# Optimization experiments

Hardware: AMD Instinct MI355X
Metric: run time of the kernel (lower is better)

Reference implementation:

```python
import jax, jax.numpy as jnp
import numpy as np

# dims: B = clips*frames, L = x spatial tokens, C = input/output/linear_out dim,
# D = conv_dim_in, NV = conv_dim_out == linear_in (visual tokens), T = num_tk
B, L, C, D, NV, T, FR = 160, 196, 768, 512, 196, 87, 10
DM, DS = C // 2, C // 16          # affine bottleneck d_model, adapter down size
ALPHA, BETA, GAMMA = 0.3, 0.05, 0.05
EPS = 1e-5


def _ln(x, g, b):
    m = x.mean(-1, keepdims=True)
    v = jnp.mean((x - m) ** 2, axis=-1, keepdims=True)
    return (x - m) * jax.lax.rsqrt(v + EPS) * g + b


def _forward(x, vis_token, conv_w, conv_b, fc_w, fc_b, my_tokens, gate_av,
             a1_w, a1_b, v1_w, v1_b, bt_w, bt_b, vc_w, vc_b, v2_w, v2_b,
             a2_w, a2_b, vs_w, vs_b, tg_w, tg_b, lnb_g, lnb_b, down_w,
             bn1_g, bn1_b, bn1_m, bn1_v, up_w, bn2_g, bn2_b, bn2_m, bn2_v,
             lnp_g, lnp_b, gate):
    vt = vis_token[..., 0]                                   # (B,NV,D)
    # conv_adapter: 1x1 conv over channel axis D -> NV, then fc over token axis NV -> C
    h = jnp.einsum('od,bnd->bon', conv_w, vt) + conv_b[None, :, None]   # (B,NV,NV)
    V = jnp.einsum('bon,cn->boc', h, fc_w) + fc_b            # (B,NV,C)  == vis_token tokens

    # token <-> visual cross-attention
    rep = jnp.broadcast_to(my_tokens, (x.shape[0], T, C))    # (B,T,C)
    att_v2tk = jax.nn.softmax(jnp.einsum('btd,bnd->btn', rep, V), axis=-1)
    rep = rep + jnp.einsum('btn,bnd->btd', att_v2tk, V)

    xt = jnp.transpose(x[..., 0], (0, 2, 1))                 # (B,L,C)
    att_tk2x = jax.nn.softmax(jnp.einsum('bld,btd->blt', xt, rep), axis=-1)
    xt = xt + gate_av * jnp.einsum('blt,btd->bld', att_tk2x, rep)

    # channel attention
    audio = V.mean(axis=1)                                   # (B,C)
    aq1 = jax.nn.relu(audio @ a1_w.T + a1_b)[:, None, :]     # (B,1,C)
    vq1 = jax.nn.relu(xt @ v1_w.T + v1_b)                    # (B,L,C)
    avq = jax.nn.relu((aq1 * vq1).mean(axis=1) @ bt_w.T + bt_b)          # (B,DM)
    ch = jax.nn.sigmoid(avq @ vc_w.T + vc_b)[:, None, :]     # (B,1,C)
    cfeat = xt * (ch + 1.0)                                  # (B,L,C)

    # spatial attention
    cq = jax.nn.relu(cfeat @ v2_w.T + v2_b)                  # (B,L,DM)
    aq2 = jax.nn.relu(audio @ a2_w.T + a2_b)[:, None, :]     # (B,1,DM)
    s_tmp = (cq * aq2) @ vs_w.T + vs_b                       # (B,L,1)
    s_sig = jax.nn.sigmoid(s_tmp)                            # (B,L,1)
    spatial = jax.nn.softmax(jnp.tanh(s_tmp).transpose(0, 2, 1), axis=-1)  # (B,1,L)

    # temporal gate over frames
    audio_r = audio.reshape(B // FR, FR, C)
    temporal = jax.nn.sigmoid(audio_r @ tg_w.T + tg_b)[..., None]          # (bs,FR,1,1)

    x5 = xt.reshape(B // FR, FR, L, C)
    factor = (ALPHA * ch.reshape(B // FR, FR, 1, C)
              + BETA * s_sig.reshape(B // FR, FR, L, 1)
              + GAMMA * temporal + (1.0 - ALPHA))
    x6 = (x5 * factor).reshape(B, L, C)

    # bottleneck adapter: LN -> down(1x1) -> BN -> ReLU -> up(1x1) -> BN -> LN -> gate
    x6 = _ln(x6, lnb_g, lnb_b)
    z = jnp.einsum('blc,oc->blo', x6, down_w)                # (B,L,DS)
    z = (z - bn1_m) * jax.lax.rsqrt(bn1_v + EPS) * bn1_g + bn1_b
    z = jax.nn.relu(z)
    o = jnp.einsum('blo,co->blc', z, up_w)                   # (B,L,C)
    o = (o - bn2_m) * jax.lax.rsqrt(bn2_v + EPS) * bn2_g + bn2_b
    o = _ln(o, lnp_g, lnp_b)
    out = (gate * o).transpose(0, 2, 1)[..., None]           # (B,C,L,1)
    return out, spatial, temporal


def setup_inputs() -> dict:
    key = jax.random.key(0)
    ks = iter(jax.random.split(key, 48))
    nrm = lambda shp, s=0.02: jax.random.normal(next(ks), shp, jnp.float32) * s
    d = {}
    d['x'] = jax.random.normal(next(ks), (B, C, L, 1), jnp.float32)
    d['vis_token'] = jax.random.normal(next(ks), (B, NV, D, 1), jnp.float32)
    d['conv_w'] = nrm((NV, D)); d['conv_b'] = jnp.zeros((NV,), jnp.float32)
    d['fc_w'] = nrm((C, NV)); d['fc_b'] = jnp.zeros((C,), jnp.float32)
    d['my_tokens'] = jax.random.uniform(next(ks), (T, C), jnp.float32)
    d['gate_av'] = jnp.float32(0.5)
    d['a1_w'] = nrm((C, C)); d['a1_b'] = jnp.zeros((C,), jnp.float32)
    d['v1_w'] = nrm((C, C)); d['v1_b'] = jnp.zeros((C,), jnp.float32)
    d['bt_w'] = nrm((DM, C)); d['bt_b'] = jnp.zeros((DM,), jnp.float32)
    d['vc_w'] = nrm((C, DM)); d['vc_b'] = jnp.zeros((C,), jnp.float32)
    d['v2_w'] = nrm((DM, C)); d['v2_b'] = jnp.zeros((DM,), jnp.float32)
    d['a2_w'] = nrm((DM, C)); d['a2_b'] = jnp.zeros((DM,), jnp.float32)
    d['vs_w'] = nrm((1, DM)); d['vs_b'] = jnp.zeros((1,), jnp.float32)
    d['tg_w'] = nrm((1, C)); d['tg_b'] = jnp.zeros((1,), jnp.float32)
    d['lnb_g'] = jnp.ones((C,), jnp.float32); d['lnb_b'] = jnp.zeros((C,), jnp.float32)
    d['down_w'] = nrm((DS, C))
    d['bn1_g'] = jnp.ones((DS,), jnp.float32); d['bn1_b'] = jnp.zeros((DS,), jnp.float32)
    d['bn1_m'] = jnp.zeros((DS,), jnp.float32); d['bn1_v'] = jnp.ones((DS,), jnp.float32)
    d['up_w'] = nrm((C, DS))
    d['bn2_g'] = jnp.ones((C,), jnp.float32); d['bn2_b'] = jnp.zeros((C,), jnp.float32)
    d['bn2_m'] = jnp.zeros((C,), jnp.float32); d['bn2_v'] = jnp.ones((C,), jnp.float32)
    d['lnp_g'] = jnp.ones((C,), jnp.float32); d['lnp_b'] = jnp.zeros((C,), jnp.float32)
    d['gate'] = jnp.float32(1.0)
    return d


def reference(x, vis_token, conv_w, conv_b, fc_w, fc_b, my_tokens, gate_av,
              a1_w, a1_b, v1_w, v1_b, bt_w, bt_b, vc_w, vc_b, v2_w, v2_b,
              a2_w, a2_b, vs_w, vs_b, tg_w, tg_b, lnb_g, lnb_b, down_w,
              bn1_g, bn1_b, bn1_m, bn1_v, up_w, bn2_g, bn2_b, bn2_m, bn2_v,
              lnp_g, lnp_b, gate):
    return _forward(x, vis_token, conv_w, conv_b, fc_w, fc_b, my_tokens, gate_av,
                    a1_w, a1_b, v1_w, v1_b, bt_w, bt_b, vc_w, vc_b, v2_w, v2_b,
                    a2_w, a2_b, vs_w, vs_b, tg_w, tg_b, lnb_g, lnb_b, down_w,
                    bn1_g, bn1_b, bn1_m, bn1_v, up_w, bn2_g, bn2_b, bn2_m, bn2_v,
                    lnp_g, lnp_b, gate)
```

## Files before the change

kernel.cpp:

```cpp
#include <hip/hip_runtime.h>
#include <math.h>

#define Bc   160
#define Lc   196
#define Cc   768
#define Dc   512
#define NVc  196
#define Tc   87
#define FRc  10
#define DMc  384
#define DSc  48
#define LROW 196
#define ALPHAc 0.3f
#define BETAc  0.05f
#define GAMMAc 0.05f
#define EPSc   1e-5f

typedef __attribute__((ext_vector_type(8))) short short8v;
typedef __attribute__((ext_vector_type(4))) short short4v;
typedef __attribute__((ext_vector_type(4))) float f32x4;

__device__ __forceinline__ short f2bf(float f) {
    unsigned u = __builtin_bit_cast(unsigned, f);
    u = (u + 0x7FFFu + ((u >> 16) & 1u)) >> 16;
    return (short)u;
}
__device__ __forceinline__ float bf2f(short s) {
    unsigned u = ((unsigned)(unsigned short)s) << 16;
    return __builtin_bit_cast(float, u);
}

__device__ __forceinline__ void gload16(const void* g, void* l) {
    using GP = const __attribute__((address_space(1))) unsigned int*;
    using LP = __attribute__((address_space(3))) unsigned int*;
    __builtin_amdgcn_global_load_lds((GP)(uintptr_t)g, (LP)(uintptr_t)l, 16, 0, 0);
}

template<int BIAS, int ACT, int OUT, int STORE, int ADDT,
         bool ASCALE, bool RSUM, bool CSCALE, bool MULP, int BMODE, bool SWZ, bool FLAT,
         bool TSTORE>
__global__ __launch_bounds__(256) void mgemm(
    const short* __restrict__ A, long sA,
    const void* __restrict__ Bp, long sB, int ldB, int Klim,
    float* __restrict__ Cf, long sCf,
    short* __restrict__ Cb, long sCb, int ldC,
    float* __restrict__ Rf, long sRf,
    const void* __restrict__ Addp, long sAdd,
    const float* __restrict__ scalePtr,
    const float* __restrict__ biasR, const float* __restrict__ biasC,
    const float* __restrict__ ascale, const float* __restrict__ wcol,
    const float* __restrict__ csc, const float* __restrict__ mulp,
    int M, int N, int K, int nI, int nJ, float outScale)
{
    __shared__ short smem[16384];
    int b, iT, jT;
    if (FLAT) {
        b = 0;
        int id = blockIdx.x;
        int nI8 = (nI >> 3) << 3;
        int main_ = nI8 * nJ;
        if (id < main_) { int xx = id & 7; int q = id >> 3; jT = q % nJ; iT = (q / nJ) * 8 + xx; }
        else { int id2 = id - main_; iT = nI8 + id2 / nJ; jT = id2 % nJ; }
    } else {
        const int tiles = nI * nJ;
        int t;
        if (SWZ) { int id = blockIdx.x; b = ((id >> 3) / tiles) * 8 + (id & 7); t = (id >> 3) % tiles; }
        else     { int id = blockIdx.x; b = id / tiles; t = id % tiles; }
        iT = t / nJ; jT = t % nJ;
    }
    const int i0 = iT * 128, j0 = jT * 128;
    const int tid = threadIdx.x;
    const int wl = tid & 63, w = tid >> 6;
    const int wr = (w >> 1) * 64, wc = (w & 1) * 64;
    const int lr = wl & 15;
    const int kgl = (((wl >> 4) ^ (lr & 3) ^ ((lr >> 2) & 3)) * 8);
    const int sl8 = (((tid & 3) ^ ((tid >> 2) & 3) ^ ((tid >> 4) & 3)) * 8);
    const int grow = w * 16 + (wl >> 2);
    const int srow = tid >> 2;
    const short* Ab = A + (FLAT ? 0L : (long)b * sA);

    f32x4 acc[4][4] = {};

    auto STAGE = [&](int bufi, int k0) {
        short* Asb = smem + bufi * 4096;
        short* Bsb = smem + 8192 + bufi * 4096;
        if (!ASCALE) {
            #pragma unroll
            for (int h = 0; h < 2; ++h) {
                int gi = i0 + h * 64 + grow; if (gi > M - 1) gi = M - 1;
                gload16(Ab + (long)gi * K + k0 + sl8, Asb + h * 2048 + w * 512);
            }
        } else {
            #pragma unroll
            for (int h = 0; h < 2; ++h) {
                int r = srow + h * 64;
                int gi = i0 + r; if (gi > M - 1) gi = M - 1;
                short8v av = *(const short8v*)(Ab + (long)gi * K + k0 + (tid & 3) * 8);
                int bb = FLAT ? (gi / LROW) : b;
                const float* asb = ascale + (long)bb * K + k0 + (tid & 3) * 8;
                #pragma unroll
                for (int e = 0; e < 8; ++e) av[e] = f2bf(bf2f(av[e]) * asb[e]);
                *(short8v*)&Asb[r * 32 + sl8] = av;
            }
        }
        if (BMODE == 0) {
            const short* Bb = (const short*)Bp + (FLAT ? 0L : (long)b * sB);
            #pragma unroll
            for (int h = 0; h < 2; ++h) {
                int gj = j0 + h * 64 + grow; if (gj > N - 1) gj = N - 1;
                gload16(Bb + (long)gj * K + k0 + sl8, Bsb + h * 2048 + w * 512);
            }
        } else if (BMODE == 2) {
            const float* Bb = (const float*)Bp + (long)b * sB;
            #pragma unroll
            for (int h = 0; h < 2; ++h) {
                int r = srow + h * 64;
                int gj = j0 + r;
                short8v bv = {};
                if (gj < N) {
                    const float* p = Bb + (long)gj * K + k0 + (tid & 3) * 8;
                    float4 lo = *(const float4*)p, hi = *(const float4*)(p + 4);
                    bv[0] = f2bf(lo.x); bv[1] = f2bf(lo.y); bv[2] = f2bf(lo.z); bv[3] = f2bf(lo.w);
                    bv[4] = f2bf(hi.x); bv[5] = f2bf(hi.y); bv[6] = f2bf(hi.z); bv[7] = f2bf(hi.w);
                }
                *(short8v*)&Bsb[r * 32 + sl8] = bv;
            }
        } else if (BMODE == 1) {
            const short* Bb = (const short*)Bp + (long)b * sB;
            #pragma unroll
            for (int h = 0; h < 2; ++h) {
                int idx = tid + h * 256;
                int kk = idx >> 4, jg = idx & 15;
                int gk = k0 + kk, gj = j0 + jg * 8;
                short8v bv = {};
                if (gk < Klim && gj < N)
                    bv = *(const short8v*)(Bb + (long)gk * ldB + gj);
                #pragma unroll
                for (int e = 0; e < 8; ++e) {
                    int row = jg * 8 + e;
                    int slot = (kk >> 3) ^ (row & 3) ^ ((row >> 2) & 3);
                    Bsb[row * 32 + slot * 8 + (kk & 7)] = bv[e];
                }
            }
        }
    };

    STAGE(0, 0);
    const int nt = K >> 5;
    for (int tt = 0; tt < nt; ++tt) {
        __syncthreads();
        if (tt + 1 < nt) STAGE((tt + 1) & 1, (tt + 1) * 32);
        const short* as = smem + (tt & 1) * 4096;
        const short* bs = smem + 8192 + (tt & 1) * 4096;
        short8v af[4], bfv[4];
        #pragma unroll
        for (int m = 0; m < 4; ++m) af[m]  = *(const short8v*)&as[(wr + m * 16 + lr) * 32 + kgl];
        #pragma unroll
        for (int n = 0; n < 4; ++n) bfv[n] = *(const short8v*)&bs[(wc + n * 16 + lr) * 32 + kgl];
        #pragma unroll
        for (int m = 0; m < 4; ++m)
            #pragma unroll
            for (int n = 0; n < 4; ++n)
                acc[m][n] = __builtin_amdgcn_mfma_f32_16x16x32_bf16(af[m], bfv[n], acc[m][n], 0, 0, 0);
    }

    const int colbase = j0 + wc;
    const int rowbase = i0 + wr;
    float scale = 1.f;
    if (ADDT) scale = scalePtr ? scalePtr[0] : 1.f;
    const int bA = FLAT ? (i0 / LROW) : 0;
    const bool straddle = FLAT && (((i0 + 127) / LROW) != bA);

    if (OUT == 0 && TSTORE) {
        float rsum[4] = {0.f, 0.f, 0.f, 0.f};
        float rsum2[4] = {0.f, 0.f, 0.f, 0.f};
        __syncthreads();
        #pragma unroll
        for (int n = 0; n < 4; ++n) {
            int col = wc + n * 16 + lr;
            int j = j0 + col;
            int jc = j < N ? j : N - 1;
            #pragma unroll
            for (int m = 0; m < 4; ++m) {
                #pragma unroll
                for (int r = 0; r < 4; ++r) {
                    int row = wr + m * 16 + (wl >> 4) * 4 + r;
                    int i = i0 + row;
                    int ic = i < M ? i : M - 1;
                    float v = acc[m][n][r];
                    if (BIAS == 1) v += biasR[ic];
                    else if (BIAS == 2) v += biasC[jc];
                    else if (BIAS == 3) v = v * biasR[jc] + biasC[jc];
                    if (ACT == 1) v = fmaxf(v, 0.f);
                    else if (ACT == 2) v = 1.f / (1.f + expf(-v));
                    else if (ACT == 3) v = 1.f + 1.f / (1.f + expf(-v));
                    if (CSCALE) v *= csc[jc];
                    if (MULP) v *= mulp[(long)ic * N + jc];
                    smem[row * 128 + col] = f2bf(v);
                    if (RSUM && j < N && i < M) {
                        if (FLAT && (i / LROW) != bA) rsum2[n] += v;
                        else rsum[n] += v;
                    }
                }
            }
        }
        if (RSUM) {
            #pragma unroll
            for (int n = 0; n < 4; ++n) {
                int j = colbase + n * 16 + lr;
                float s = rsum[n];
                s += __shfl_xor(s, 16, 64);
                s += __shfl_xor(s, 32, 64);
                float s2 = 0.f;
                if (FLAT && straddle) {
                    s2 = rsum2[n];
                    s2 += __shfl_xor(s2, 16, 64);
                    s2 += __shfl_xor(s2, 32, 64);
                }
                if ((wl >> 4) == 0 && j < N) {
                    atomicAdd(&Rf[(long)bA * sRf + (FLAT ? 0 : (long)b * sRf) + j], s * outScale);
                    if (FLAT && straddle)
                        atomicAdd(&Rf[(long)(bA + 1) * sRf + j], s2 * outScale);
                }
            }
        }
        __syncthreads();
        #pragma unroll
        for (int p = 0; p < 8; ++p) {
            int row = (tid >> 4) + p * 16;
            int i = i0 + row;
            int c8 = (tid & 15) * 8;
            int j = j0 + c8;
            if (i < M && j < ldC) {
                short8v sv = *(const short8v*)&smem[row * 128 + c8];
                if (ADDT == 2) {
                    const short* ap = (const short*)Addp + (long)b * sAdd + (long)i * N + j;
                    short8v av = *(const short8v*)ap;
                    #pragma unroll
                    for (int e = 0; e < 8; ++e) sv[e] = f2bf(bf2f(av[e]) + scale * bf2f(sv[e]));
                } else if (ADDT == 1) {
                    const float* ap = (const float*)Addp + (long)b * sAdd + (long)i * N + j;
                    f32x4 lo = *(const f32x4*)ap, hi = *(const f32x4*)(ap + 4);
                    #pragma unroll
                    for (int e = 0; e < 4; ++e) sv[e] = f2bf(lo[e] + scale * bf2f(sv[e]));
                    #pragma unroll
                    for (int e = 0; e < 4; ++e) sv[e + 4] = f2bf(hi[e] + scale * bf2f(sv[e + 4]));
                }
                *(short8v*)&Cb[(long)b * sCb + (long)i * ldC + j] = sv;
            }
        }
    } else if (OUT == 0) {
        float rsum[4] = {0.f, 0.f, 0.f, 0.f};
        float rsum2[4] = {0.f, 0.f, 0.f, 0.f};
        #pragma unroll
        for (int n = 0; n < 4; ++n) {
            int j = colbase + n * 16 + lr;
            if (j >= N) continue;
            #pragma unroll
            for (int m = 0; m < 4; ++m) {
                #pragma unroll
                for (int r = 0; r < 4; ++r) {
                    int i = rowbase + m * 16 + (wl >> 4) * 4 + r;
                    if (i >= M) continue;
                    float v = acc[m][n][r];
                    if (BIAS == 1) v += biasR[i];
                    else if (BIAS == 2) v += biasC[j];
                    else if (BIAS == 3) v = v * biasR[j] + biasC[j];
                    if (ACT == 1) v = fmaxf(v, 0.f);
                    else if (ACT == 2) v = 1.f / (1.f + expf(-v));
                    else if (ACT == 3) v = 1.f + 1.f / (1.f + expf(-v));
                    if (CSCALE) v *= csc[j];
                    if (MULP) v *= mulp[(long)i * N + j];
                    if (ADDT == 1) v = ((const float*)Addp)[(long)b * sAdd + (long)i * N + j] + scale * v;
                    else if (ADDT == 2) v = bf2f(((const short*)Addp)[(long)b * sAdd + (long)i * N + j]) + scale * v;
                    if (STORE & 1) Cf[(long)b * sCf + (long)i * N + j] = v;
                    if (STORE & 2) Cb[(long)b * sCb + (long)i * ldC + j] = f2bf(v);
                    if (RSUM) {
                        if (FLAT && (i / LROW) != bA) rsum2[n] += v;
                        else rsum[n] += v;
                    }
                }
            }
        }
        if (RSUM) {
            #pragma unroll
            for (int n = 0; n < 4; ++n) {
                int j = colbase + n * 16 + lr;
                float s = rsum[n];
                s += __shfl_xor(s, 16, 64);
                s += __shfl_xor(s, 32, 64);
                float s2 = 0.f;
                if (FLAT && straddle) {
                    s2 = rsum2[n];
                    s2 += __shfl_xor(s2, 16, 64);
                    s2 += __shfl_xor(s2, 32, 64);
                }
                if ((wl >> 4) == 0 && j < N) {
                    atomicAdd(&Rf[(long)bA * sRf + (FLAT ? 0 : (long)b * sRf) + j], s * outScale);
                    if (FLAT && straddle)
                        atomicAdd(&Rf[(long)(bA + 1) * sRf + j], s2 * outScale);
                }
            }
        }
    } else if (OUT == 1) {
        #pragma unroll
        for (int n = 0; n < 4; ++n) {
            int j = colbase + n * 16 + lr;
            if (j < N) {
                float s = 0.f, s2 = 0.f;
                #pragma unroll
                for (int m = 0; m < 4; ++m)
                    #pragma unroll
                    for (int r = 0; r < 4; ++r) {
                        int i = rowbase + m * 16 + (wl >> 4) * 4 + r;
                        if (i >= M) continue;
                        float v = acc[m][n][r];
                        if (BIAS == 2) v += biasC[j];
                        if (ACT == 1) v = fmaxf(v, 0.f);
                        if (FLAT && (i / LROW) != bA) s2 += v; else s += v;
                    }
                s += __shfl_xor(s, 16, 64);
                s += __shfl_xor(s, 32, 64);
                if (FLAT && straddle) {
                    s2 += __shfl_xor(s2, 16, 64);
                    s2 += __shfl_xor(s2, 32, 64);
                }
                if ((wl >> 4) == 0) {
                    atomicAdd(&Cf[(long)(FLAT ? bA : b) * sCf + j], s * outScale);
                    if (FLAT && straddle)
                        atomicAdd(&Cf[(long)(bA + 1) * sCf + j], s2 * outScale);
                }
            }
        }
    } else {
        #pragma unroll
        for (int m = 0; m < 4; ++m) {
            #pragma unroll
            for (int r = 0; r < 4; ++r) {
                int i = rowbase + m * 16 + (wl >> 4) * 4 + r;
                int bw = FLAT ? (i < M ? i / LROW : 0) : b;
                float s = 0.f;
                #pragma unroll
                for (int n = 0; n < 4; ++n) {
                    int j = colbase + n * 16 + lr;
                    if (j >= N) continue;
                    float v = acc[m][n][r];
                    if (BIAS == 2) v += biasC[j];
                    if (ACT == 1) v = fmaxf(v, 0.f);
                    s += v * wcol[(long)bw * N + j];
                }
                s += __shfl_xor(s, 1, 64);
                s += __shfl_xor(s, 2, 64);
                s += __shfl_xor(s, 4, 64);
                s += __shfl_xor(s, 8, 64);
                if (lr == 0 && i < M)
                    atomicAdd(&Cf[(FLAT ? (long)i : (long)b * sCf + i)], s * outScale);
            }
        }
    }
}

__global__ void k_cvt_weights(
    const float* __restrict__ my_tok, const float* __restrict__ conv_w,
    const float* __restrict__ a1_w, const float* __restrict__ v1_w,
    const float* __restrict__ bt_w, const float* __restrict__ vc_w,
    const float* __restrict__ v2_w, const float* __restrict__ a2_w,
    const float* __restrict__ down_w, const float* __restrict__ fc_w,
    const float* __restrict__ up_w,
    short* __restrict__ mytok_bf, short* __restrict__ wconv,
    short* __restrict__ wa1, short* __restrict__ wv1,
    short* __restrict__ wbt, short* __restrict__ wvc,
    short* __restrict__ wv2, short* __restrict__ wa2,
    short* __restrict__ wdown, short* __restrict__ wfc, short* __restrict__ wup)
{
    long idx = (long)blockIdx.x * 256 + threadIdx.x;
    if (idx < 66816)  { mytok_bf[idx] = f2bf(my_tok[idx]); return; }  idx -= 66816;
    if (idx < 100352) { wconv[idx] = f2bf(conv_w[idx]); return; }     idx -= 100352;
    if (idx < 589824) { wa1[idx] = f2bf(a1_w[idx]); return; }         idx -= 589824;
    if (idx < 589824) { wv1[idx] = f2bf(v1_w[idx]); return; }         idx -= 589824;
    if (idx < 294912) { wbt[idx] = f2bf(bt_w[idx]); return; }         idx -= 294912;
    if (idx < 294912) { wvc[idx] = f2bf(vc_w[idx]); return; }         idx -= 294912;
    if (idx < 294912) { wv2[idx] = f2bf(v2_w[idx]); return; }         idx -= 294912;
    if (idx < 294912) { wa2[idx] = f2bf(a2_w[idx]); return; }         idx -= 294912;
    if (idx < 36864)  { wdown[idx] = f2bf(down_w[idx]); return; }     idx -= 36864;
    if (idx < 172032) { int r = (int)(idx / 224), c = (int)(idx % 224);
                        wfc[idx] = (c < 196) ? f2bf(fc_w[(long)r * 196 + c]) : (short)0; return; }
    idx -= 172032;
    if (idx < 49152)  { int r = (int)(idx / 64), c = (int)(idx % 64);
                        wup[idx] = (c < 48) ? f2bf(up_w[(long)r * 48 + c]) : (short)0; }
}

__global__ void k_prep(const float* g1, const float* b1, const float* m1, const float* v1,
                       const float* g2, const float* b2, const float* m2, const float* v2,
                       float* scl1, float* sft1, float* scl2, float* sft2)
{
    int j = threadIdx.x;
    if (j < DSc) { float r = rsqrtf(v1[j] + EPSc) * g1[j]; scl1[j] = r; sft1[j] = b1[j] - m1[j] * r; }
    if (j < Cc)  { float r = rsqrtf(v2[j] + EPSc) * g2[j]; scl2[j] = r; sft2[j] = b2[j] - m2[j] * r; }
}

__global__ __launch_bounds__(256) void k_transpose(const float* __restrict__ x, short* __restrict__ xtb)
{
    __shared__ float tile[64][33];
    int b = blockIdx.z;
    int c0 = blockIdx.y * 64, l0 = blockIdx.x * 32;
    int tx = threadIdx.x & 31, ty = threadIdx.x >> 5;
    #pragma unroll
    for (int k = 0; k < 8; ++k) {
        int c = c0 + ty + 8 * k, l = l0 + tx;
        tile[ty + 8 * k][tx] = (l < Lc) ? x[((long)b * Cc + c) * Lc + l] : 0.f;
    }
    __syncthreads();
    int cg = threadIdx.x & 15, lw = threadIdx.x >> 4;
    #pragma unroll
    for (int p = 0; p < 2; ++p) {
        int l = l0 + lw + p * 16;
        if (l >= Lc) continue;
        int c = c0 + cg * 4;
        short4v sv;
        #pragma unroll
        for (int e = 0; e < 4; ++e) sv[e] = f2bf(tile[cg * 4 + e][lw + p * 16]);
        *(short4v*)(xtb + ((long)b * Lc + l) * Cc + c) = sv;
    }
}

__global__ __launch_bounds__(256) void k_audio_fin(
    const float* __restrict__ audio, short* __restrict__ audio_bf,
    const float* __restrict__ tg_w, const float* __restrict__ tg_b,
    float* __restrict__ tempv, float* __restrict__ outTemp)
{
    __shared__ float red[256];
    int b = blockIdx.x, tid = threadIdx.x;
    float part = 0.f;
    #pragma unroll
    for (int q = 0; q < 3; ++q) {
        int c = tid + q * 256;
        float a = audio[(long)b * Cc + c];
        audio_bf[(long)b * Cc + c] = f2bf(a);
        part += a * tg_w[c];
    }
    red[tid] = part; __syncthreads();
    for (int s = 128; s > 0; s >>= 1) { if (tid < s) red[tid] += red[tid + s]; __syncthreads(); }
    if (tid == 0) {
        float t = 1.f / (1.f + expf(-(red[0] + tg_b[0])));
        tempv[b] = t; outTemp[b] = t;
    }
}

__global__ __launch_bounds__(256) void k_softmax_w(const float* __restrict__ in,
                                                   short* __restrict__ out,
                                                   int n, int ldo, int rows)
{
    int r = blockIdx.x * 4 + (threadIdx.x >> 6);
    int lane = threadIdx.x & 63;
    if (r >= rows) return;
    const float* row = in + (long)r * n;
    float v[4];
    float mx = -INFINITY;
    #pragma unroll
    for (int q = 0; q < 4; ++q) {
        int c = lane + q * 64;
        v[q] = (c < n) ? row[c] : -INFINITY;
        mx = fmaxf(mx, v[q]);
    }
    #pragma unroll
    for (int off = 32; off > 0; off >>= 1) mx = fmaxf(mx, __shfl_xor(mx, off, 64));
    float sum = 0.f;
    #pragma unroll
    for (int q = 0; q < 4; ++q) {
        int c = lane + q * 64;
        float e = (c < n) ? expf(v[q] - mx) : 0.f;
        v[q] = e; sum += e;
    }
    #pragma unroll
    for (int off = 32; off > 0; off >>= 1) sum += __shfl_xor(sum, off, 64);
    float inv = 1.0f / sum;
    #pragma unroll
    for (int q = 0; q < 4; ++q) {
        int c = lane + q * 64;
        if (c < ldo) out[(long)r * ldo + c] = (c < n) ? f2bf(v[q] * inv) : (short)0;
    }
}

__global__ __launch_bounds__(256) void k_spatial(const float* __restrict__ stmp,
                                                 const float* __restrict__ vs_b,
                                                 float* __restrict__ ssig,
                                                 float* __restrict__ spat)
{
    __shared__ float red[256];
    int b = blockIdx.x, tid = threadIdx.x;
    float t = -INFINITY;
    if (tid < Lc) {
        float v = stmp[(long)b * Lc + tid] + vs_b[0];
        ssig[(long)b * Lc + tid] = 1.f / (1.f + expf(-v));
        t = tanhf(v);
    }
    red[tid] = t; __syncthreads();
    for (int s = 128; s > 0; s >>= 1) { if (tid < s) red[tid] = fmaxf(red[tid], red[tid + s]); __syncthreads(); }
    float mx = red[0]; __syncthreads();
    float e = (tid < Lc) ? expf(t - mx) : 0.f;
    red[tid] = e; __syncthreads();
    for (int s = 128; s > 0; s >>= 1) { if (tid < s) red[tid] += red[tid + s]; __syncthreads(); }
    if (tid < Lc) spat[(long)b * Lc + tid] = e / red[0];
}

__global__ __launch_bounds__(256) void k_ln_factor(
    short* __restrict__ xt, const float* __restrict__ chp1,
    const float* __restrict__ ssig, const float* __restrict__ tmp_,
    const float* __restrict__ g, const float* __restrict__ be)
{
    long r = (long)blockIdx.x * 4 + (threadIdx.x >> 6);
    int lane = threadIdx.x & 63;
    int b = (int)(r / Lc);
    float rowterm = BETAc * ssig[r] + GAMMAc * tmp_[b] + (1.0f - ALPHAc);
    float v[12];
    #pragma unroll
    for (int q = 0; q < 3; ++q) {
        int c = lane * 4 + q * 256;
        short4v sv = *(const short4v*)(xt + r * Cc + c);
        f32x4 ch = *(const f32x4*)(chp1 + (long)b * Cc + c);
        #pragma unroll
        for (int e = 0; e < 4; ++e)
            v[q * 4 + e] = bf2f(sv[e]) * (ALPHAc * (ch[e] - 1.0f) + rowterm);
    }
    float s = 0.f;
    #pragma unroll
    for (int e = 0; e < 12; ++e) s += v[e];
    #pragma unroll
    for (int off = 32; off > 0; off >>= 1) s += __shfl_xor(s, off, 64);
    float mean = s * (1.0f / Cc);
    float var = 0.f;
    #pragma unroll
    for (int e = 0; e < 12; ++e) { float d = v[e] - mean; var += d * d; }
    #pragma unroll
    for (int off = 32; off > 0; off >>= 1) var += __shfl_xor(var, off, 64);
    float rs = rsqrtf(var * (1.0f / Cc) + EPSc);
    #pragma unroll
    for (int q = 0; q < 3; ++q) {
        int c = lane * 4 + q * 256;
        f32x4 gv = *(const f32x4*)(g + c);
        f32x4 bv = *(const f32x4*)(be + c);
        short4v sv;
        #pragma unroll
        for (int e = 0; e < 4; ++e)
            sv[e] = f2bf((v[q * 4 + e] - mean) * rs * gv[e] + bv[e]);
        *(short4v*)(xt + r * Cc + c) = sv;
    }
}

__global__ __launch_bounds__(256) void k_final(
    const short* __restrict__ o,
    const float* __restrict__ lng, const float* __restrict__ lnb,
    const float* __restrict__ gatePtr, float* __restrict__ out)
{
    __shared__ short ot[16 * 776];
    __shared__ float mean_s[16], rsv_s[16];
    int lt = blockIdx.x, b = blockIdx.y;
    int l0 = lt * 16;
    int tid = threadIdx.x;
    int rows = Lc - l0; if (rows > 16) rows = 16;
    const short* src = o + ((long)b * Lc + l0) * Cc;
    int n8 = rows * 96;
    for (int idx = tid; idx < n8; idx += 256) {
        int rr = idx / 96, c8 = idx % 96;
        short8v val = *(const short8v*)(src + (long)rr * Cc + c8 * 8);
        *(short8v*)&ot[rr * 776 + c8 * 8] = val;
    }
    __syncthreads();
    int w = tid >> 6, lane = tid & 63;
    for (int rr = w; rr < rows; rr += 4) {
        float v[12];
        #pragma unroll
        for (int q = 0; q < 3; ++q) {
            int c = lane * 4 + q * 256;
            short4v sv = *(const short4v*)&ot[rr * 776 + c];
            #pragma unroll
            for (int e = 0; e < 4; ++e) v[q * 4 + e] = bf2f(sv[e]);
        }
        float s = 0.f;
        #pragma unroll
        for (int e = 0; e < 12; ++e) s += v[e];
        #pragma unroll
        for (int off = 32; off > 0; off >>= 1) s += __shfl_xor(s, off, 64);
        float mean = s * (1.0f / Cc);
        float var = 0.f;
        #pragma unroll
        for (int e = 0; e < 12; ++e) { float d = v[e] - mean; var += d * d; }
        #pragma unroll
        for (int off = 32; off > 0; off >>= 1) var += __shfl_xor(var, off, 64);
        if (lane == 0) {
            mean_s[rr] = mean;
            rsv_s[rr] = rsqrtf(var * (1.0f / Cc) + EPSc);
        }
    }
    __syncthreads();
    float gate = gatePtr[0];
    if (rows == 16) {
        for (int idx = tid; idx < Cc * 4; idx += 256) {
            int c = idx >> 2, q = idx & 3;
            float lg = lng[c], lb = lnb[c];
            f32x4 val;
            #pragma unroll
            for (int e = 0; e < 4; ++e) {
                int rr = q * 4 + e;
                float xv = bf2f(ot[rr * 776 + c]);
                val[e] = gate * ((xv - mean_s[rr]) * rsv_s[rr] * lg + lb);
            }
            *(f32x4*)(out + ((long)b * Cc + c) * Lc + l0 + q * 4) = val;
        }
    } else {
        for (int idx = tid; idx < Cc; idx += 256) {
            int c = idx;
            float lg = lng[c], lb = lnb[c];
            f32x4 val;
            #pragma unroll
            for (int e = 0; e < 4; ++e) {
                float xv = bf2f(ot[e * 776 + c]);
                val[e] = gate * ((xv - mean_s[e]) * rsv_s[e] * lg + lb);
            }
            *(f32x4*)(out + ((long)b * Cc + c) * Lc + l0) = val;
        }
    }
}

extern "C" void kernel_launch(void* const* d_in, const int* in_sizes, int n_in,
                              void* d_out, int out_size, void* d_ws, size_t ws_size,
                              hipStream_t stream)
{
    const float* x       = (const float*)d_in[0];
    const float* vis     = (const float*)d_in[1];
    const float* conv_w  = (const float*)d_in[2];
    const float* conv_b  = (const float*)d_in[3];
    const float* fc_w    = (const float*)d_in[4];
    const float* fc_b    = (const float*)d_in[5];
    const float* my_tok  = (const float*)d_in[6];
    const float* gate_av = (const float*)d_in[7];
    const float* a1_w    = (const float*)d_in[8];
    const float* a1_b    = (const float*)d_in[9];
    const float* v1_w    = (const float*)d_in[10];
    const float* v1_b    = (const float*)d_in[11];
    const float* bt_w    = (const float*)d_in[12];
    const float* bt_b    = (const float*)d_in[13];
    const float* vc_w    = (const float*)d_in[14];
    const float* vc_b    = (const float*)d_in[15];
    const float* v2_w    = (const float*)d_in[16];
    const float* v2_b    = (const float*)d_in[17];
    const float* a2_w    = (const float*)d_in[18];
    const float* a2_b    = (const float*)d_in[19];
    const float* vs_w    = (const float*)d_in[20];
    const float* vs_b    = (const float*)d_in[21];
    const float* tg_w    = (const float*)d_in[22];
    const float* tg_b    = (const float*)d_in[23];
    const float* lnb_g   = (const float*)d_in[24];
    const float* lnb_b   = (const float*)d_in[25];
    const float* down_w  = (const float*)d_in[26];
    const float* bn1_g   = (const float*)d_in[27];
    const float* bn1_b   = (const float*)d_in[28];
    const float* bn1_m   = (const float*)d_in[29];
    const float* bn1_v   = (const float*)d_in[30];
    const float* up_w    = (const float*)d_in[31];
    const float* bn2_g   = (const float*)d_in[32];
    const float* bn2_b   = (const float*)d_in[33];
    const float* bn2_m   = (const float*)d_in[34];
    const float* bn2_v   = (const float*)d_in[35];
    const float* lnp_g   = (const float*)d_in[36];
    const float* lnp_b   = (const float*)d_in[37];
    const float* gate    = (const float*)d_in[38];

    float* out = (float*)d_out;
    float* outSpat = out + (long)Bc * Cc * Lc;
    float* outTemp = outSpat + (long)Bc * Lc;

    float* wsf   = (float*)d_ws;
    float* scoresf = wsf;
    float* audio = scoresf + 2729280L;
    float* vq1m  = audio + 122880L;
    float* stmp  = vq1m + 122880L;
    float* chp1  = stmp + 31360L;
    float* aq2   = chp1 + 122880L;
    float* ssig  = aq2 + 61440L;
    float* tempv = ssig + 31360L;
    float* bnscl1 = tempv + 192L;
    float* bnsft1 = bnscl1 + 64L;
    float* bnscl2 = bnsft1 + 64L;
    float* bnsft2 = bnscl2 + 768L;
    short* wss   = (short*)(bnsft2 + 768L);
    short* P2    = wss;
    short* P3    = P2 + 24084480L;
    short* P4    = P3 + 10690560L;
    short* zb_bf = P4 + 3118080L;
    short* audio_bf = zb_bf + 2007040L;
    short* avqin_bf = audio_bf + 122880L;
    short* avq_bf   = avqin_bf + 122880L;
    short* mytok_bf = avq_bf + 61440L;
    short* wconv = mytok_bf + 66816L;
    short* wa1   = wconv + 100352L;
    short* wv1   = wa1 + 589824L;
    short* wbt   = wv1 + 589824L;
    short* wvc   = wbt + 294912L;
    short* wv2   = wvc + 294912L;
    short* wa2   = wv2 + 294912L;
    short* wdown = wa2 + 294912L;
    short* wfc   = wdown + 36864L;
    short* wup   = wfc + 172032L;

    dim3 blk(256);
    auto cgrid = [](long n) { return dim3((unsigned)((n + 255) / 256)); };
    const int MF = Bc * Lc;

    k_cvt_weights<<<cgrid(2784512L), blk, 0, stream>>>(
        my_tok, conv_w, a1_w, v1_w, bt_w, vc_w, v2_w, a2_w, down_w, fc_w, up_w,
        mytok_bf, wconv, wa1, wv1, wbt, wvc, wv2, wa2, wdown, wfc, wup);
    k_prep<<<1, 768, 0, stream>>>(bn1_g, bn1_b, bn1_m, bn1_v,
                                  bn2_g, bn2_b, bn2_m, bn2_v,
                                  bnscl1, bnsft1, bnscl2, bnsft2);
    hipMemsetAsync(audio, 0, (size_t)(122880 + 122880 + 31360) * sizeof(float), stream);

    mgemm<1,0,0,2,0,false,false,false,false,2,true,false,true><<<dim3(160*4), blk, 0, stream>>>(
        wconv, 0, vis, (long)NVc*Dc, 0, Dc, nullptr, 0, P3, (long)NVc*224, 224,
        nullptr, 0, nullptr, 0, nullptr, conv_b, nullptr, nullptr, nullptr, nullptr, nullptr,
        NVc, NVc, Dc, 2, 2, 1.f);

    mgemm<2,0,0,2,0,false,true,false,false,0,false,true,true><<<dim3(245*6), blk, 0, stream>>>(
        P3, 0, wfc, 0, 0, 224, nullptr, 0, P2, 0, Cc,
        audio, Cc, nullptr, 0, nullptr, nullptr, fc_b, nullptr, nullptr, nullptr, nullptr,
        MF, Cc, 224, 245, 6, 1.0f/NVc);

    k_audio_fin<<<dim3(Bc), blk, 0, stream>>>(audio, audio_bf, tg_w, tg_b, tempv, outTemp);

    mgemm<0,0,0,1,0,false,false,false,false,0,true,false,false><<<dim3(160*2), blk, 0, stream>>>(
        mytok_bf, 0, P2, (long)NVc*Cc, 0, Cc, scoresf, (long)Tc*NVc, nullptr, 0, 0,
        nullptr, 0, nullptr, 0, nullptr, nullptr, nullptr, nullptr, nullptr, nullptr, nullptr,
        Tc, NVc, Cc, 1, 2, 1.f);

    k_softmax_w<<<dim3((Bc*Tc+3)/4), blk, 0, stream>>>(scoresf, P4, NVc, 224, Bc*Tc);

    mgemm<0,0,0,2,1,false,false,false,false,1,true,false,true><<<dim3(160*6), blk, 0, stream>>>(
        P4, (long)Tc*224, P2, (long)NVc*Cc, Cc, NVc, nullptr, 0, P3, (long)Tc*Cc, Cc,
        nullptr, 0, my_tok, 0, nullptr, nullptr, nullptr, nullptr, nullptr, nullptr, nullptr,
        Tc, Cc, 224, 1, 6, 1.f);

    k_transpose<<<dim3(7,12,Bc), blk, 0, stream>>>(x, P2);

    mgemm<0,0,0,1,0,false,false,false,false,0,true,false,false><<<dim3(160*2), blk, 0, stream>>>(
        P2, (long)Lc*Cc, P3, (long)Tc*Cc, 0, Cc, scoresf, (long)Lc*Tc, nullptr, 0, 0,
        nullptr, 0, nullptr, 0, nullptr, nullptr, nullptr, nullptr, nullptr, nullptr, nullptr,
        Lc, Tc, Cc, 2, 1, 1.f);

    k_softmax_w<<<dim3((Bc*Lc+3)/4), blk, 0, stream>>>(scoresf, P4, Tc, 96, Bc*Lc);

    mgemm<0,0,0,2,2,false,false,false,false,1,true,false,true><<<dim3(160*12), blk, 0, stream>>>(
        P4, (long)Lc*96, P3, (long)Tc*Cc, Cc, Tc, nullptr, 0, P2, (long)Lc*Cc, Cc,
        nullptr, 0, P2, (long)Lc*Cc, gate_av, nullptr, nullptr, nullptr, nullptr, nullptr, nullptr,
        Lc, Cc, 96, 2, 6, 1.f);

    mgemm<2,1,1,0,0,false,false,false,false,0,false,true,false><<<dim3(245*6), blk, 0, stream>>>(
        P2, 0, wv1, 0, 0, Cc, vq1m, Cc, nullptr, 0, 0,
        nullptr, 0, nullptr, 0, nullptr, nullptr, v1_b, nullptr, nullptr, nullptr, nullptr,
        MF, Cc, Cc, 245, 6, 1.0f/Lc);

    mgemm<2,1,0,2,0,false,false,false,true,0,false,false,true><<<dim3(12), blk, 0, stream>>>(
        audio_bf, 0, wa1, 0, 0, Cc, nullptr, 0, avqin_bf, 0, Cc,
        nullptr, 0, nullptr, 0, nullptr, nullptr, a1_b, nullptr, nullptr, nullptr, vq1m,
        Bc, Cc, Cc, 2, 6, 1.f);

    mgemm<2,1,0,2,0,false,false,false,false,0,false,false,true><<<dim3(6), blk, 0, stream>>>(
        avqin_bf, 0, wbt, 0, 0, Cc, nullptr, 0, avq_bf, 0, DMc,
        nullptr, 0, nullptr, 0, nullptr, nullptr, bt_b, nullptr, nullptr, nullptr, nullptr,
        Bc, DMc, Cc, 2, 3, 1.f);

    mgemm<2,3,0,1,0,false,false,false,false,0,false,false,false><<<dim3(12), blk, 0, stream>>>(
        avq_bf, 0, wvc, 0, 0, DMc, chp1, 0, nullptr, 0, 0,
        nullptr, 0, nullptr, 0, nullptr, nullptr, vc_b, nullptr, nullptr, nullptr, nullptr,
        Bc, Cc, DMc, 2, 6, 1.f);

    mgemm<2,1,0,1,0,false,false,true,false,0,false,false,false><<<dim3(6), blk, 0, stream>>>(
        audio_bf, 0, wa2, 0, 0, Cc, aq2, 0, nullptr, 0, 0,
        nullptr, 0, nullptr, 0, nullptr, nullptr, a2_b, nullptr, nullptr, vs_w, nullptr,
        Bc, DMc, Cc, 2, 3, 1.f);

    mgemm<2,1,2,0,0,true,false,false,false,0,false,true,false><<<dim3(245*3), blk, 0, stream>>>(
        P2, 0, wv2, 0, 0, Cc, stmp, 0, nullptr, 0, 0,
        nullptr, 0, nullptr, 0, nullptr, nullptr, v2_b, chp1, aq2, nullptr, nullptr,
        MF, DMc, Cc, 245, 3, 1.f);

    k_spatial<<<dim3(Bc), blk, 0, stream>>>(stmp, vs_b, ssig, outSpat);

    k_ln_factor<<<dim3(Bc*Lc/4), blk, 0, stream>>>(
        P2, chp1, ssig, tempv, lnb_g, lnb_b);

    mgemm<3,1,0,2,0,false,false,false,false,0,false,true,true><<<dim3(245), blk, 0, stream>>>(
        P2, 0, wdown, 0, 0, Cc, nullptr, 0, zb_bf, 0, 64,
        nullptr, 0, nullptr, 0, nullptr, bnscl1, bnsft1, nullptr, nullptr, nullptr, nullptr,
        MF, DSc, Cc, 245, 1, 1.f);

    mgemm<3,0,0,2,0,false,false,false,false,0,false,true,true><<<dim3(245*6), blk, 0, stream>>>(
        zb_bf, 0, wup, 0, 0, 64, nullptr, 0, P2, 0, Cc,
        nullptr, 0, nullptr, 0, nullptr, bnscl2, bnsft2, nullptr, nullptr, nullptr, nullptr,
        MF, Cc, 64, 245, 6, 1.f);

    k_final<<<dim3(13,Bc), blk, 0, stream>>>(
        P2, lnp_g, lnp_b, gate, out);
}
```

Measured before the change: 561.3 us.

## Add triple-buffered LDS pipeline with partial vmcnt waits for direct-load GEMMs

For GEMM variants whose A and B tiles are loaded straight to LDS (BMODE 0, no A scaling), the shared buffer grows to three stages. Loads are issued two K-tiles ahead, and the wait uses s_waitcnt vmcnt(4) plus a raw barrier, so each wait covers only the oldest tile's loads. The goal is to hide global-load latency behind MFMA work instead of draining every load each iteration. It costs 50% more LDS for those variants, which may lower occupancy, and it depends on the exact count of outstanding loads per stage being correct.

```diff
diff --git a/kernel.cpp b/kernel.cpp
--- a/kernel.cpp
+++ b/kernel.cpp
@@ -52,7 +52,10 @@
     const float* __restrict__ csc, const float* __restrict__ mulp,
     int M, int N, int K, int nI, int nJ, float outScale)
 {
-    __shared__ short smem[16384];
+    constexpr bool DEEP = (BMODE == 0) && !ASCALE;
+    constexpr int LDSN = DEEP ? 24576 : 16384;
+    constexpr int BOFF = DEEP ? 12288 : 8192;
+    __shared__ short smem[LDSN];
     int b, iT, jT;
     if (FLAT) {
         b = 0;
@@ -81,9 +84,7 @@
 
     f32x4 acc[4][4] = {};
 
-    auto STAGE = [&](int bufi, int k0) {
-        short* Asb = smem + bufi * 4096;
-        short* Bsb = smem + 8192 + bufi * 4096;
+    auto STAGE = [&](short* Asb, short* Bsb, int k0) {
         if (!ASCALE) {
             #pragma unroll
             for (int h = 0; h < 2; ++h) {
@@ -145,13 +146,7 @@
         }
     };
 
-    STAGE(0, 0);
-    const int nt = K >> 5;
-    for (int tt = 0; tt < nt; ++tt) {
-        __syncthreads();
-        if (tt + 1 < nt) STAGE((tt + 1) & 1, (tt + 1) * 32);
-        const short* as = smem + (tt & 1) * 4096;
-        const short* bs = smem + 8192 + (tt & 1) * 4096;
+    auto COMPUTE = [&](const short* as, const short* bs) {
         short8v af[4], bfv[4];
         #pragma unroll
         for (int m = 0; m < 4; ++m) af[m]  = *(const short8v*)&as[(wr + m * 16 + lr) * 32 + kgl];
@@ -162,6 +157,35 @@
             #pragma unroll
             for (int n = 0; n < 4; ++n)
                 acc[m][n] = __builtin_amdgcn_mfma_f32_16x16x32_bf16(af[m], bfv[n], acc[m][n], 0, 0, 0);
+    };
+
+    const int nt = K >> 5;
+    if (DEEP) {
+        STAGE(smem, smem + BOFF, 0);
+        if (nt > 1) STAGE(smem + 4096, smem + BOFF + 4096, 32);
+        for (int tt = 0; tt < nt; ++tt) {
+            if (tt + 1 < nt) asm volatile("s_waitcnt vmcnt(4)" ::: "memory");
+            else             asm volatile("s_waitcnt vmcnt(0)" ::: "memory");
+            __builtin_amdgcn_s_barrier();
+            __builtin_amdgcn_sched_barrier(0);
+            if (tt + 2 < nt) {
+                int nb = (tt + 2) % 3;
+                STAGE(smem + nb * 4096, smem + BOFF + nb * 4096, (tt + 2) * 32);
+            }
+            int cb = tt % 3;
+            COMPUTE(smem + cb * 4096, smem + BOFF + cb * 4096);
+        }
+    } else {
+        STAGE(smem, smem + BOFF, 0);
+        for (int tt = 0; tt < nt; ++tt) {
+            __syncthreads();
+            if (tt + 1 < nt) {
+                int nb = (tt + 1) & 1;
+                STAGE(smem + nb * 4096, smem + BOFF + nb * 4096, (tt + 1) * 32);
+            }
+            int cb = tt & 1;
+            COMPUTE(smem + cb * 4096, smem + BOFF + cb * 4096);
+        }
     }
 
     const int colbase = j0 + wc;
```

Result: no change. 550.4 us (-1.9%).
